# Kernel optimization log

Hardware: AMD Instinct MI355X
Metric: run time of the kernel (lower is better)

The kernel has to match this reference:

```python
import jax, jax.numpy as jnp
import numpy as np

D_MODEL = 768
N_HEADS = 12
HEAD_DIM = D_MODEL // N_HEADS
B, T = 2, 2048


def setup_inputs() -> dict:
    key = jax.random.key(0)
    k1, k2, k3 = jax.random.split(key, 3)
    x = jax.random.normal(k1, (B, T, D_MODEL), dtype=jnp.float32)
    # causal mask: positions where mask == 0 (False) get -inf
    mask = jnp.tril(jnp.ones((T, T), dtype=bool))[None, None, :, :]
    Wqkv = jax.random.normal(k2, (D_MODEL, 3 * D_MODEL), dtype=jnp.float32) * (D_MODEL ** -0.5)
    bqkv = jnp.zeros((3 * D_MODEL,), dtype=jnp.float32)
    Wout = jax.random.normal(k3, (D_MODEL, D_MODEL), dtype=jnp.float32) * (D_MODEL ** -0.5)
    bout = jnp.zeros((D_MODEL,), dtype=jnp.float32)
    return {"x": x, "mask": mask, "Wqkv": Wqkv, "bqkv": bqkv, "Wout": Wout, "bout": bout}


def reference(x, mask, Wqkv, bqkv, Wout, bout):
    b, t, c = x.shape
    qkv = x @ Wqkv + bqkv                      # [B, T, 3C]
    q, k, v = jnp.split(qkv, 3, axis=-1)
    def heads(z):  # [B, T, C] -> [B, H, T, Dh]
        return z.reshape(b, t, N_HEADS, HEAD_DIM).transpose(0, 2, 1, 3)
    q, k, v = heads(q), heads(k), heads(v)
    scores = jnp.einsum('bhqd,bhkd->bhqk', q, k) / jnp.sqrt(jnp.float32(HEAD_DIM))
    scores = jnp.where(mask, scores, -jnp.inf)
    attn = jax.nn.softmax(scores, axis=-1)
    out = jnp.einsum('bhqk,bhkd->bhqd', attn, v)  # [B, H, T, Dh]
    out = out.transpose(0, 2, 1, 3).reshape(b, t, c)
    # dropout is identity in eval mode
    return out @ Wout + bout
```

## Files before the change

kernel.cpp:

```cpp
#include <hip/hip_runtime.h>
#include <math.h>

#define BB 2
#define TT 2048
#define CC 768
#define HH 12
#define DD 64
#define MROWS (BB*TT)
#define NQKV (3*CC)
#define QBLK 64

typedef short bf16x8 __attribute__((ext_vector_type(8)));
typedef float f32x4 __attribute__((ext_vector_type(4)));

__device__ __forceinline__ unsigned short f2bf(float f) {
    union { float f; unsigned u; } v; v.f = f;
    unsigned u = v.u + 0x7FFF + ((v.u >> 16) & 1);
    return (unsigned short)(u >> 16);
}

__device__ __forceinline__ unsigned cvtpk_bf16(float lo, float hi) {
    unsigned r;
    asm("v_cvt_pk_bf16_f32 %0, %1, %2" : "=v"(r) : "v"(lo), "v"(hi));
    return r;
}

__device__ __forceinline__ void gload_lds16(const void* g, void* l) {
    __builtin_amdgcn_global_load_lds(
        (const __attribute__((address_space(1))) unsigned int*)g,
        (__attribute__((address_space(3))) unsigned int*)l, 16, 0, 0);
}

#define XBLOCKS 512
#define TQKV_TILES ((NQKV/64)*(CC/64))
#define TOUT_TILES ((CC/64)*(CC/64))

__global__ __launch_bounds__(256) void prep(const float* __restrict__ x,
                                            const float* __restrict__ Wqkv,
                                            const float* __restrict__ Wout,
                                            unsigned short* __restrict__ xb,
                                            unsigned short* __restrict__ wqkv_t,
                                            unsigned short* __restrict__ wout_t)
{
    int bid = blockIdx.x;
    if (bid < XBLOCKS) {
        const int total8 = MROWS * CC / 8;
        for (int i = bid * 256 + threadIdx.x; i < total8; i += XBLOCKS * 256) {
            float4 a = ((const float4*)x)[i * 2];
            float4 b = ((const float4*)x)[i * 2 + 1];
            ushort4 lo = { f2bf(a.x), f2bf(a.y), f2bf(a.z), f2bf(a.w) };
            ushort4 hi = { f2bf(b.x), f2bf(b.y), f2bf(b.z), f2bf(b.w) };
            ((ushort4*)xb)[i * 2]     = lo;
            ((ushort4*)xb)[i * 2 + 1] = hi;
        }
        return;
    }
    bid -= XBLOCKS;
    const float* src; unsigned short* dst; int srcN, nt, kt;
    if (bid < TQKV_TILES) { src = Wqkv; dst = wqkv_t; srcN = NQKV;
                            nt = bid % (NQKV/64); kt = bid / (NQKV/64); }
    else { bid -= TQKV_TILES; src = Wout; dst = wout_t; srcN = CC;
           nt = bid % (CC/64); kt = bid / (CC/64); }

    __shared__ float Ts[64][65];
    const int n0 = nt * 64, k0 = kt * 64;
#pragma unroll
    for (int p = 0; p < 4; ++p) {
        int c = p * 256 + threadIdx.x;
        int row = c >> 4, col4 = c & 15;
        float4 v = *(const float4*)&src[(size_t)(k0 + row) * srcN + n0 + col4 * 4];
        Ts[row][col4 * 4 + 0] = v.x;
        Ts[row][col4 * 4 + 1] = v.y;
        Ts[row][col4 * 4 + 2] = v.z;
        Ts[row][col4 * 4 + 3] = v.w;
    }
    __syncthreads();
#pragma unroll
    for (int p = 0; p < 4; ++p) {
        int t = p * 256 + threadIdx.x;
        int on = t >> 4, oslot = t & 15;
        ushort4 o = { f2bf(Ts[oslot * 4 + 0][on]), f2bf(Ts[oslot * 4 + 1][on]),
                      f2bf(Ts[oslot * 4 + 2][on]), f2bf(Ts[oslot * 4 + 3][on]) };
        *(ushort4*)&dst[(size_t)(n0 + on) * CC + k0 + oslot * 4] = o;
    }
}

__global__ __launch_bounds__(256) void qkv_mfma(const unsigned short* __restrict__ A,
                                                const unsigned short* __restrict__ Bt,
                                                const float* __restrict__ bias,
                                                unsigned short* __restrict__ qb,
                                                unsigned short* __restrict__ kb,
                                                unsigned short* __restrict__ vb)
{
    __shared__ unsigned short As[64 * 64];
    __shared__ unsigned short Bs[128 * 64];
    const int tid = threadIdx.x;
    const int wv = tid >> 6, l = tid & 63, g = l >> 4, lr = l & 15;
    const int wm = wv >> 1, wn = wv & 1;
    const int GX = NQKV / 128;
    const int nwg = GX * (MROWS / 64);
    int lin = blockIdx.y * GX + blockIdx.x;
    int swz = (lin & 7) * (nwg >> 3) + (lin >> 3);
    const int m0 = (swz / GX) * 64, n0 = (swz % GX) * 128;
    const int h7 = lr & 7;

    f32x4 acc[2][4] = {};

    for (int k0 = 0; k0 < CC; k0 += 64) {
        __syncthreads();
#pragma unroll
        for (int p = 0; p < 2; ++p) {
            int c = p * 256 + tid;
            int row = c >> 3, slot = c & 7;
            int ss = slot ^ (row & 7);
            gload_lds16(A + (size_t)(m0 + row) * CC + k0 + ss * 8, As + c * 8);
        }
#pragma unroll
        for (int p = 0; p < 4; ++p) {
            int c = p * 256 + tid;
            int row = c >> 3, slot = c & 7;
            int ss = slot ^ (row & 7);
            gload_lds16(Bt + (size_t)(n0 + row) * CC + k0 + ss * 8, Bs + c * 8);
        }
        __syncthreads();
        bf16x8 af[2][2], bfr[4][2];
#pragma unroll
        for (int i = 0; i < 2; ++i)
#pragma unroll
            for (int kt = 0; kt < 2; ++kt) {
                int row = wm * 32 + i * 16 + lr;
                af[i][kt] = *(const bf16x8*)&As[row * 64 + ((kt * 4 + g) ^ h7) * 8];
            }
#pragma unroll
        for (int j = 0; j < 4; ++j)
#pragma unroll
            for (int kt = 0; kt < 2; ++kt) {
                int row = wn * 64 + j * 16 + lr;
                bfr[j][kt] = *(const bf16x8*)&Bs[row * 64 + ((kt * 4 + g) ^ h7) * 8];
            }
#pragma unroll
        for (int i = 0; i < 2; ++i)
#pragma unroll
            for (int j = 0; j < 4; ++j)
#pragma unroll
                for (int kt = 0; kt < 2; ++kt)
                    acc[i][j] = __builtin_amdgcn_mfma_f32_16x16x32_bf16(af[i][kt], bfr[j][kt], acc[i][j], 0, 0, 0);
    }

#pragma unroll
    for (int i = 0; i < 2; ++i)
#pragma unroll
        for (int r = 0; r < 4; ++r) {
            int m = m0 + wm * 32 + i * 16 + 4 * g + r;
            int b_ = m >> 11, t = m & (TT - 1);
#pragma unroll
            for (int j = 0; j < 4; ++j) {
                int n = n0 + wn * 64 + j * 16 + lr;
                float val = acc[i][j][r] + bias[n];
                int which = n / CC;
                int rr = n - which * CC;
                int h = rr >> 6, d = rr & 63;
                size_t bh = (size_t)b_ * HH + h;
                if (which == 0)      qb[(bh * TT + t) * DD + d] = f2bf(val * 0.18033688f);
                else if (which == 1) kb[(bh * TT + t) * DD + d] = f2bf(val);
                else                 vb[(bh * DD + d) * TT + t] = f2bf(val);
            }
        }
}

__global__ __launch_bounds__(256) void out_mfma(const unsigned short* __restrict__ A,
                                                const unsigned short* __restrict__ Bt,
                                                const float* __restrict__ bias,
                                                float* __restrict__ out)
{
    __shared__ unsigned short As[64 * 64];
    __shared__ unsigned short Bs[64 * 64];
    const int tid = threadIdx.x;
    const int wv = tid >> 6, l = tid & 63, g = l >> 4, lr = l & 15;
    const int wm = wv >> 1, wn = wv & 1;
    const int GX = CC / 64;
    const int nwg = GX * (MROWS / 64);
    int lin = blockIdx.y * GX + blockIdx.x;
    int swz = (lin & 7) * (nwg >> 3) + (lin >> 3);
    const int m0 = (swz / GX) * 64, n0 = (swz % GX) * 64;
    const int h7 = lr & 7;

    f32x4 acc[2][2] = {};

    for (int k0 = 0; k0 < CC; k0 += 64) {
        __syncthreads();
#pragma unroll
        for (int p = 0; p < 2; ++p) {
            int c = p * 256 + tid;
            int row = c >> 3, slot = c & 7;
            int ss = slot ^ (row & 7);
            gload_lds16(A  + (size_t)(m0 + row) * CC + k0 + ss * 8, As + c * 8);
            gload_lds16(Bt + (size_t)(n0 + row) * CC + k0 + ss * 8, Bs + c * 8);
        }
        __syncthreads();
        bf16x8 af[2][2], bfr[2][2];
#pragma unroll
        for (int i = 0; i < 2; ++i)
#pragma unroll
            for (int kt = 0; kt < 2; ++kt) {
                int arow = wm * 32 + i * 16 + lr;
                af[i][kt] = *(const bf16x8*)&As[arow * 64 + ((kt * 4 + g) ^ h7) * 8];
                int brow = wn * 32 + i * 16 + lr;
                bfr[i][kt] = *(const bf16x8*)&Bs[brow * 64 + ((kt * 4 + g) ^ h7) * 8];
            }
#pragma unroll
        for (int i = 0; i < 2; ++i)
#pragma unroll
            for (int j = 0; j < 2; ++j)
#pragma unroll
                for (int kt = 0; kt < 2; ++kt)
                    acc[i][j] = __builtin_amdgcn_mfma_f32_16x16x32_bf16(af[i][kt], bfr[j][kt], acc[i][j], 0, 0, 0);
    }

#pragma unroll
    for (int i = 0; i < 2; ++i)
#pragma unroll
        for (int r = 0; r < 4; ++r) {
            int m = m0 + wm * 32 + i * 16 + 4 * g + r;
#pragma unroll
            for (int j = 0; j < 2; ++j) {
                int n = n0 + wn * 32 + j * 16 + lr;
                out[(size_t)m * CC + n] = acc[i][j][r] + bias[n];
            }
        }
}

__global__ __launch_bounds__(256) void attn_mfma(
    const unsigned short* __restrict__ qb,
    const unsigned short* __restrict__ kb,
    const unsigned short* __restrict__ vtb,
    unsigned short* __restrict__ outp)
{
    __shared__ unsigned short Ks[2 * 64 * 64];
    __shared__ unsigned short Vts[2 * 64 * 64];

    const int blk  = blockIdx.x;
    const int head = blk % (BB * HH);
    const int qt   = (TT / QBLK - 1) - blk / (BB * HH);
    const int tid  = threadIdx.x;
    const int wv   = tid >> 6;
    const int l    = tid & 63;
    const int g    = l >> 4;
    const int lr   = l & 15;

    const size_t hb = (size_t)head * TT * DD;
    const int qrow0 = qt * QBLK + wv * 16;

    bf16x8 qf[2];
#pragma unroll
    for (int dt = 0; dt < 2; ++dt)
        qf[dt] = *(const bf16x8*)(qb + hb + (size_t)(qrow0 + lr) * DD + dt * 32 + 8 * g);

    f32x4 oacc[4] = {};
    float lpart = 0.f;

    const int srow0 = tid >> 3, srow1 = srow0 + 32;
    const int slot  = tid & 7;
#define RHO(k) ((((k) >> 5) << 5) | ((((k) >> 2) & 1) << 4) | ((((k) >> 3) & 3) << 2) | ((k) & 3))
    const int rho0 = RHO(srow0), rho1 = RHO(srow1);
    const int koff0 = (rho0 * 64 + slot * 8) ^ ((rho0 & 7) << 3);
    const int koff1 = (rho1 * 64 + slot * 8) ^ ((rho1 & 7) << 3);
    const int voff0 = (srow0 * 64 + slot * 8) ^ ((srow0 & 7) << 3);
    const int voff1 = (srow1 * 64 + slot * 8) ^ ((srow1 & 7) << 3);
    const unsigned short* kg0 = kb  + hb + (size_t)srow0 * DD + slot * 8;
    const unsigned short* kg1 = kb  + hb + (size_t)srow1 * DD + slot * 8;
    const unsigned short* vg0 = vtb + hb + (size_t)srow0 * TT + slot * 8;
    const unsigned short* vg1 = vtb + hb + (size_t)srow1 * TT + slot * 8;

    *(bf16x8*)&Ks[koff0]  = *(const bf16x8*)(kg0);
    *(bf16x8*)&Ks[koff1]  = *(const bf16x8*)(kg1);
    *(bf16x8*)&Vts[voff0] = *(const bf16x8*)(vg0);
    *(bf16x8*)&Vts[voff1] = *(const bf16x8*)(vg1);
    __syncthreads();

    int bo = 0;
    for (int c = 0; c <= qt; ++c) {
        const bool more = (c < qt);
        bf16x8 nk0, nk1, nv0, nv1;
        if (more) {
            nk0 = *(const bf16x8*)(kg0 + (size_t)(c + 1) * 64 * DD);
            nk1 = *(const bf16x8*)(kg1 + (size_t)(c + 1) * 64 * DD);
            nv0 = *(const bf16x8*)(vg0 + (c + 1) * 64);
            nv1 = *(const bf16x8*)(vg1 + (c + 1) * 64);
        }

        f32x4 sacc[4] = {};
        __builtin_amdgcn_s_setprio(1);
#pragma unroll
        for (int jt = 0; jt < 4; ++jt) {
#pragma unroll
            for (int dt = 0; dt < 2; ++dt) {
                int prow = jt * 16 + lr;
                int off = bo + ((prow * 64 + dt * 32 + g * 8) ^ ((prow & 7) << 3));
                bf16x8 kf = *(const bf16x8*)&Ks[off];
                sacc[jt] = __builtin_amdgcn_mfma_f32_16x16x32_bf16(kf, qf[dt], sacc[jt], 0, 0, 0);
            }
        }
        __builtin_amdgcn_s_setprio(0);

        float pv[4][4];
        const int qloc = wv * 16 + lr;
        const bool diag = (c == qt);
#pragma unroll
        for (int jt = 0; jt < 4; ++jt)
#pragma unroll
            for (int r = 0; r < 4; ++r) {
                float p = __builtin_amdgcn_exp2f(sacc[jt][r]);
                if (diag) {
                    int keyl = 32 * (jt >> 1) + 8 * g + 4 * (jt & 1) + r;
                    if (keyl > qloc) p = 0.f;
                }
                pv[jt][r] = p;
                lpart += p;
            }

        union { bf16x8 v; unsigned u[4]; } pf0, pf1;
        pf0.u[0] = cvtpk_bf16(pv[0][0], pv[0][1]);
        pf0.u[1] = cvtpk_bf16(pv[0][2], pv[0][3]);
        pf0.u[2] = cvtpk_bf16(pv[1][0], pv[1][1]);
        pf0.u[3] = cvtpk_bf16(pv[1][2], pv[1][3]);
        pf1.u[0] = cvtpk_bf16(pv[2][0], pv[2][1]);
        pf1.u[1] = cvtpk_bf16(pv[2][2], pv[2][3]);
        pf1.u[2] = cvtpk_bf16(pv[3][0], pv[3][1]);
        pf1.u[3] = cvtpk_bf16(pv[3][2], pv[3][3]);

        __builtin_amdgcn_s_setprio(1);
#pragma unroll
        for (int dt = 0; dt < 4; ++dt) {
#pragma unroll
            for (int kt = 0; kt < 2; ++kt) {
                int row = dt * 16 + lr;
                int off = bo + ((row * 64 + kt * 32 + g * 8) ^ ((row & 7) << 3));
                bf16x8 vf = *(const bf16x8*)&Vts[off];
                oacc[dt] = __builtin_amdgcn_mfma_f32_16x16x32_bf16(
                    kt ? pf1.v : pf0.v, vf, oacc[dt], 0, 0, 0);
            }
        }
        __builtin_amdgcn_s_setprio(0);

        if (more) {
            int nb = bo ^ (64 * 64);
            *(bf16x8*)&Ks[nb + koff0]  = nk0;
            *(bf16x8*)&Ks[nb + koff1]  = nk1;
            *(bf16x8*)&Vts[nb + voff0] = nv0;
            *(bf16x8*)&Vts[nb + voff1] = nv1;
            __syncthreads();
            bo = nb;
        }
    }

    float lsum = lpart;
    lsum += __shfl_xor(lsum, 16);
    lsum += __shfl_xor(lsum, 32);
    float linv[4];
#pragma unroll
    for (int r = 0; r < 4; ++r)
        linv[r] = 1.f / __shfl(lsum, 4 * g + r);

    const int b_ = head / HH, h = head % HH;
#pragma unroll
    for (int dt = 0; dt < 4; ++dt)
#pragma unroll
        for (int r = 0; r < 4; ++r) {
            int qg = qrow0 + 4 * g + r;
            outp[((size_t)b_ * TT + qg) * CC + h * DD + dt * 16 + lr] =
                f2bf(oacc[dt][r] * linv[r]);
        }
}

extern "C" void kernel_launch(void* const* d_in, const int* in_sizes, int n_in,
                              void* d_out, int out_size, void* d_ws, size_t ws_size,
                              hipStream_t stream)
{
    const float* x    = (const float*)d_in[0];
    const float* Wqkv = (const float*)d_in[2];
    const float* bqkv = (const float*)d_in[3];
    const float* Wout = (const float*)d_in[4];
    const float* bout = (const float*)d_in[5];
    float* out = (float*)d_out;

    unsigned short* p = (unsigned short*)d_ws;
    unsigned short* xb      = p;  p += (size_t)MROWS * CC;
    unsigned short* wqkv_t  = p;  p += (size_t)NQKV * CC;
    unsigned short* wout_t  = p;  p += (size_t)CC * CC;
    unsigned short* qb      = p;  p += (size_t)BB * HH * TT * DD;
    unsigned short* kb      = p;  p += (size_t)BB * HH * TT * DD;
    unsigned short* vb      = p;  p += (size_t)BB * HH * TT * DD;
    unsigned short* attnb   = p;  p += (size_t)MROWS * CC;

    prep<<<XBLOCKS + TQKV_TILES + TOUT_TILES, 256, 0, stream>>>(x, Wqkv, Wout, xb, wqkv_t, wout_t);

    dim3 g1(NQKV / 128, MROWS / 64);
    qkv_mfma<<<g1, 256, 0, stream>>>(xb, wqkv_t, bqkv, qb, kb, vb);

    dim3 g2(BB * HH * (TT / QBLK));
    attn_mfma<<<g2, 256, 0, stream>>>(qb, kb, vb, attnb);

    dim3 g3(CC / 64, MROWS / 64);
    out_mfma<<<g3, 256, 0, stream>>>(attnb, wout_t, bout, out);
}
```

Before: 164.8 us.

## Process 128 query rows per attention block and remap blocks to XCDs by head

Each attention workgroup now handles a 128-row query tile, with each wave owning two 16-row groups. Every K/V tile loaded into LDS is therefore reused for twice as many query rows, which halves K/V global traffic and barrier count per query row. Block indices are also remapped so consecutive blocks on the same XCD share a head, for L2 locality. In exchange the grid shrinks to 384 blocks, the causal work imbalance gets coarser, and register pressure roughly doubles for the accumulators.

```diff
diff --git a/kernel.cpp b/kernel.cpp
--- a/kernel.cpp
+++ b/kernel.cpp
@@ -8,7 +8,6 @@
 #define DD 64
 #define MROWS (BB*TT)
 #define NQKV (3*CC)
-#define QBLK 64
 
 typedef short bf16x8 __attribute__((ext_vector_type(8)));
 typedef float f32x4 __attribute__((ext_vector_type(4)));
@@ -240,8 +239,10 @@
     __shared__ unsigned short Vts[2 * 64 * 64];
 
     const int blk  = blockIdx.x;
-    const int head = blk % (BB * HH);
-    const int qt   = (TT / QBLK - 1) - blk / (BB * HH);
+    const int xcd  = blk & 7;
+    const int wq   = blk >> 3;
+    const int head = xcd + 8 * (wq % 3);
+    const int qt   = 15 - wq / 3;
     const int tid  = threadIdx.x;
     const int wv   = tid >> 6;
     const int l    = tid & 63;
@@ -249,15 +250,17 @@
     const int lr   = l & 15;
 
     const size_t hb = (size_t)head * TT * DD;
-    const int qrow0 = qt * QBLK + wv * 16;
-
-    bf16x8 qf[2];
-#pragma unroll
-    for (int dt = 0; dt < 2; ++dt)
-        qf[dt] = *(const bf16x8*)(qb + hb + (size_t)(qrow0 + lr) * DD + dt * 32 + 8 * g);
-
-    f32x4 oacc[4] = {};
-    float lpart = 0.f;
+    const int qrow0 = qt * 128 + wv * 32;
+
+    bf16x8 qf[2][2];
+#pragma unroll
+    for (int rg = 0; rg < 2; ++rg)
+#pragma unroll
+        for (int dt = 0; dt < 2; ++dt)
+            qf[rg][dt] = *(const bf16x8*)(qb + hb + (size_t)(qrow0 + rg * 16 + lr) * DD + dt * 32 + 8 * g);
+
+    f32x4 oacc[2][4] = {};
+    float lpart0 = 0.f, lpart1 = 0.f;
 
     const int srow0 = tid >> 3, srow1 = srow0 + 32;
     const int slot  = tid & 7;
@@ -278,9 +281,10 @@
     *(bf16x8*)&Vts[voff1] = *(const bf16x8*)(vg1);
     __syncthreads();
 
+    const int nch = 2 * qt + 2;
     int bo = 0;
-    for (int c = 0; c <= qt; ++c) {
-        const bool more = (c < qt);
+    for (int c = 0; c < nch; ++c) {
+        const bool more = (c + 1 < nch);
         bf16x8 nk0, nk1, nv0, nv1;
         if (more) {
             nk0 = *(const bf16x8*)(kg0 + (size_t)(c + 1) * 64 * DD);
@@ -289,7 +293,7 @@
             nv1 = *(const bf16x8*)(vg1 + (c + 1) * 64);
         }
 
-        f32x4 sacc[4] = {};
+        f32x4 sacc0[4] = {}, sacc1[4] = {};
         __builtin_amdgcn_s_setprio(1);
 #pragma unroll
         for (int jt = 0; jt < 4; ++jt) {
@@ -298,36 +302,47 @@
                 int prow = jt * 16 + lr;
                 int off = bo + ((prow * 64 + dt * 32 + g * 8) ^ ((prow & 7) << 3));
                 bf16x8 kf = *(const bf16x8*)&Ks[off];
-                sacc[jt] = __builtin_amdgcn_mfma_f32_16x16x32_bf16(kf, qf[dt], sacc[jt], 0, 0, 0);
+                sacc0[jt] = __builtin_amdgcn_mfma_f32_16x16x32_bf16(kf, qf[0][dt], sacc0[jt], 0, 0, 0);
+                sacc1[jt] = __builtin_amdgcn_mfma_f32_16x16x32_bf16(kf, qf[1][dt], sacc1[jt], 0, 0, 0);
             }
         }
         __builtin_amdgcn_s_setprio(0);
 
-        float pv[4][4];
-        const int qloc = wv * 16 + lr;
-        const bool diag = (c == qt);
+        float pv0[4][4], pv1[4][4];
+        const bool diag = (c >= 2 * qt);
+        const int qg0 = qrow0 + lr;
 #pragma unroll
         for (int jt = 0; jt < 4; ++jt)
 #pragma unroll
             for (int r = 0; r < 4; ++r) {
-                float p = __builtin_amdgcn_exp2f(sacc[jt][r]);
+                float p0 = __builtin_amdgcn_exp2f(sacc0[jt][r]);
+                float p1 = __builtin_amdgcn_exp2f(sacc1[jt][r]);
                 if (diag) {
-                    int keyl = 32 * (jt >> 1) + 8 * g + 4 * (jt & 1) + r;
-                    if (keyl > qloc) p = 0.f;
+                    int keyg = c * 64 + 32 * (jt >> 1) + 8 * g + 4 * (jt & 1) + r;
+                    if (keyg > qg0)      p0 = 0.f;
+                    if (keyg > qg0 + 16) p1 = 0.f;
                 }
-                pv[jt][r] = p;
-                lpart += p;
-            }
-
-        union { bf16x8 v; unsigned u[4]; } pf0, pf1;
-        pf0.u[0] = cvtpk_bf16(pv[0][0], pv[0][1]);
-        pf0.u[1] = cvtpk_bf16(pv[0][2], pv[0][3]);
-        pf0.u[2] = cvtpk_bf16(pv[1][0], pv[1][1]);
-        pf0.u[3] = cvtpk_bf16(pv[1][2], pv[1][3]);
-        pf1.u[0] = cvtpk_bf16(pv[2][0], pv[2][1]);
-        pf1.u[1] = cvtpk_bf16(pv[2][2], pv[2][3]);
-        pf1.u[2] = cvtpk_bf16(pv[3][0], pv[3][1]);
-        pf1.u[3] = cvtpk_bf16(pv[3][2], pv[3][3]);
+                pv0[jt][r] = p0; lpart0 += p0;
+                pv1[jt][r] = p1; lpart1 += p1;
+            }
+
+        union { bf16x8 v; unsigned u[4]; } pa0, pa1, pb0, pb1;
+        pa0.u[0] = cvtpk_bf16(pv0[0][0], pv0[0][1]);
+        pa0.u[1] = cvtpk_bf16(pv0[0][2], pv0[0][3]);
+        pa0.u[2] = cvtpk_bf16(pv0[1][0], pv0[1][1]);
+        pa0.u[3] = cvtpk_bf16(pv0[1][2], pv0[1][3]);
+        pa1.u[0] = cvtpk_bf16(pv0[2][0], pv0[2][1]);
+        pa1.u[1] = cvtpk_bf16(pv0[2][2], pv0[2][3]);
+        pa1.u[2] = cvtpk_bf16(pv0[3][0], pv0[3][1]);
+        pa1.u[3] = cvtpk_bf16(pv0[3][2], pv0[3][3]);
+        pb0.u[0] = cvtpk_bf16(pv1[0][0], pv1[0][1]);
+        pb0.u[1] = cvtpk_bf16(pv1[0][2], pv1[0][3]);
+        pb0.u[2] = cvtpk_bf16(pv1[1][0], pv1[1][1]);
+        pb0.u[3] = cvtpk_bf16(pv1[1][2], pv1[1][3]);
+        pb1.u[0] = cvtpk_bf16(pv1[2][0], pv1[2][1]);
+        pb1.u[1] = cvtpk_bf16(pv1[2][2], pv1[2][3]);
+        pb1.u[2] = cvtpk_bf16(pv1[3][0], pv1[3][1]);
+        pb1.u[3] = cvtpk_bf16(pv1[3][2], pv1[3][3]);
 
         __builtin_amdgcn_s_setprio(1);
 #pragma unroll
@@ -337,8 +352,10 @@
                 int row = dt * 16 + lr;
                 int off = bo + ((row * 64 + kt * 32 + g * 8) ^ ((row & 7) << 3));
                 bf16x8 vf = *(const bf16x8*)&Vts[off];
-                oacc[dt] = __builtin_amdgcn_mfma_f32_16x16x32_bf16(
-                    kt ? pf1.v : pf0.v, vf, oacc[dt], 0, 0, 0);
+                oacc[0][dt] = __builtin_amdgcn_mfma_f32_16x16x32_bf16(
+                    kt ? pa1.v : pa0.v, vf, oacc[0][dt], 0, 0, 0);
+                oacc[1][dt] = __builtin_amdgcn_mfma_f32_16x16x32_bf16(
+                    kt ? pb1.v : pb0.v, vf, oacc[1][dt], 0, 0, 0);
             }
         }
         __builtin_amdgcn_s_setprio(0);
@@ -354,22 +371,26 @@
         }
     }
 
-    float lsum = lpart;
-    lsum += __shfl_xor(lsum, 16);
-    lsum += __shfl_xor(lsum, 32);
-    float linv[4];
-#pragma unroll
-    for (int r = 0; r < 4; ++r)
-        linv[r] = 1.f / __shfl(lsum, 4 * g + r);
+    float ls0 = lpart0, ls1 = lpart1;
+    ls0 += __shfl_xor(ls0, 16); ls0 += __shfl_xor(ls0, 32);
+    ls1 += __shfl_xor(ls1, 16); ls1 += __shfl_xor(ls1, 32);
+    float linv0[4], linv1[4];
+#pragma unroll
+    for (int r = 0; r < 4; ++r) {
+        linv0[r] = 1.f / __shfl(ls0, 4 * g + r);
+        linv1[r] = 1.f / __shfl(ls1, 4 * g + r);
+    }
 
     const int b_ = head / HH, h = head % HH;
 #pragma unroll
     for (int dt = 0; dt < 4; ++dt)
 #pragma unroll
         for (int r = 0; r < 4; ++r) {
-            int qg = qrow0 + 4 * g + r;
-            outp[((size_t)b_ * TT + qg) * CC + h * DD + dt * 16 + lr] =
-                f2bf(oacc[dt][r] * linv[r]);
+            int q0 = qrow0 + 4 * g + r;
+            outp[((size_t)b_ * TT + q0) * CC + h * DD + dt * 16 + lr] =
+                f2bf(oacc[0][dt][r] * linv0[r]);
+            outp[((size_t)b_ * TT + q0 + 16) * CC + h * DD + dt * 16 + lr] =
+                f2bf(oacc[1][dt][r] * linv1[r]);
         }
 }
 
@@ -398,7 +419,7 @@
     dim3 g1(NQKV / 128, MROWS / 64);
     qkv_mfma<<<g1, 256, 0, stream>>>(xb, wqkv_t, bqkv, qb, kb, vb);
 
-    dim3 g2(BB * HH * (TT / QBLK));
+    dim3 g2(8 * 3 * (TT / 128));
     attn_mfma<<<g2, 256, 0, stream>>>(qb, kb, vb, attnb);
 
     dim3 g3(CC / 64, MROWS / 64);
```

New measurement: 177.6 us. 1.08x slower.
